# Performance work log

Hardware: AMD Instinct MI355X
Metric: run time of the kernel (lower is better)

## Reference

```python
import jax, jax.numpy as jnp
import numpy as np

B, LQ, S, D, H = 8, 1024, 256, 1024, 16
HD = D // H
LN_EPS = 1e-5


def layer_norm(x, g, b):
    m = jnp.mean(x, axis=-1, keepdims=True)
    v = jnp.mean((x - m) ** 2, axis=-1, keepdims=True)
    return (x - m) / jnp.sqrt(v + LN_EPS) * g + b


def setup_inputs() -> dict:
    key = jax.random.key(0)
    ks = jax.random.split(key, 12)
    sc = 0.02
    p = lambda k, shp: jax.random.normal(k, shp, dtype=jnp.float32) * sc
    return {
        "memory": jax.random.normal(ks[0], (B, LQ, D // 2), dtype=jnp.float32),
        "gaze_features": jax.random.normal(ks[1], (B, LQ, D // 2), dtype=jnp.float32),
        "text_features": jax.random.normal(ks[2], (B, S, D), dtype=jnp.float32),
        "w_in": p(ks[3], (3 * D, D)),  # packed q,k,v in_proj (torch MHA layout)
        "b_in": jnp.zeros((3 * D,), jnp.float32),
        "w_o": p(ks[4], (D, D)),
        "b_o": jnp.zeros((D,), jnp.float32),
        "w1": p(ks[5], (D, D)),
        "b1": jnp.zeros((D,), jnp.float32),
        "w2": p(ks[6], (D, D)),
        "b2": jnp.zeros((D,), jnp.float32),
        "g1": jnp.ones((D,), jnp.float32),
        "be1": jnp.zeros((D,), jnp.float32),
        "g2": jnp.ones((D,), jnp.float32),
        "be2": jnp.zeros((D,), jnp.float32),
    }


def reference(memory, gaze_features, text_features, w_in, b_in, w_o, b_o,
              w1, b1, w2, b2, g1, be1, g2, be2):
    combined = jnp.concatenate([memory, gaze_features], axis=-1)  # [B, LQ, D]
    wq, wk, wv = w_in[:D], w_in[D:2 * D], w_in[2 * D:]
    bq, bk, bv = b_in[:D], b_in[D:2 * D], b_in[2 * D:]

    q = (combined @ wq.T + bq).reshape(B, LQ, H, HD)
    k = (text_features @ wk.T + bk).reshape(B, S, H, HD)
    v = (text_features @ wv.T + bv).reshape(B, S, H, HD)

    scores = jnp.einsum("bqhd,bkhd->bhqk", q, k) / jnp.sqrt(jnp.float32(HD))
    attn_w = jax.nn.softmax(scores, axis=-1)
    ctx = jnp.einsum("bhqk,bkhd->bqhd", attn_w, v).reshape(B, LQ, D)
    attn_output = ctx @ w_o.T + b_o  # [B, LQ, D]

    # dual FFN branches share linear1/linear2 (as in the source); dropout = eval identity
    ffn = jax.nn.relu(attn_output @ w1.T + b1) @ w2.T + b2
    refpoint_embed = layer_norm(ffn, g1, be1)
    tgt = layer_norm(ffn, g2, be2)

    # vectorized box decode (replaces the per-element Python loop)
    s = jax.nn.sigmoid(attn_output[..., :4])
    xc, yc, w, h = s[..., 0], s[..., 1], s[..., 2], s[..., 3]
    init_box_proposal = jnp.stack(
        [xc - w / 2, yc - h / 2, xc + w / 2, yc + h / 2], axis=-1)  # [B, LQ, 4]

    return refpoint_embed, tgt, init_box_proposal
```

## Files before the change

kernel.cpp:

```cpp
#include <hip/hip_runtime.h>


typedef unsigned short u16;
typedef unsigned int u32;
typedef __bf16 bf16x8 __attribute__((ext_vector_type(8)));
typedef float f32x4 __attribute__((ext_vector_type(4)));
typedef u16 u16x4 __attribute__((ext_vector_type(4)));

struct CvtArgs { const void* in[15]; };

__device__ __forceinline__ u16 f2bf(float f) {
  u32 u = __builtin_bit_cast(u32, f);
  u += 0x7fffu + ((u >> 16) & 1u);
  return (u16)(u >> 16);
}
__device__ __forceinline__ float bf2f(u16 h) {
  u32 u = ((u32)h) << 16;
  return __builtin_bit_cast(float, u);
}

struct WsPtrs {
  u16 *c_mem, *c_gaze, *c_text, *c_win, *c_bin, *c_wo, *c_bo, *c_w1, *c_b1,
      *c_w2, *c_b2, *c_g1, *c_be1, *c_g2, *c_be2;
  u16 *q, *k, *v, *ctx, *woT, *wf, *bfb, *h1, *ffnb;
};
__device__ __forceinline__ WsPtrs wsp(u16* C) {
  WsPtrs w;
  w.c_mem = C;                 w.c_gaze = C + 4194304;   w.c_text = C + 8388608;
  w.c_win = C + 10485760;      w.c_bin = C + 13631488;   w.c_wo = C + 13634560;
  w.c_bo = C + 14683136;       w.c_w1 = C + 14684160;    w.c_b1 = C + 15732736;
  w.c_w2 = C + 15733760;       w.c_b2 = C + 16782336;    w.c_g1 = C + 16783360;
  w.c_be1 = C + 16784384;      w.c_g2 = C + 16785408;    w.c_be2 = C + 16786432;
  u16* B2 = C + 16787488;
  w.q = B2;                    w.k = B2 + 8388608;       w.v = B2 + 10485760;
  w.ctx = B2 + 12582912;
  w.woT = B2 + 20971520;
  w.wf  = B2 + 22020096;
  w.bfb = B2 + 23068672;
  w.h1  = B2 + 29360128;
  w.ffnb = B2;
  return w;
}

__device__ __forceinline__ void cvt_chunk(bool f32in, u16* dst,
                                          const void* const* srcs, u32 c8) {
  const u32 cum[16] = {0u, 4194304u, 8388608u, 10485760u, 13631488u, 13634560u,
                       14683136u, 14684160u, 15732736u, 15733760u, 16782336u,
                       16783360u, 16784384u, 16785408u, 16786432u, 16787456u};
  u32 base = c8 * 8u;
  int idx = 0;
#pragma unroll
  for (int i = 1; i < 15; ++i) if (base >= cum[i]) idx = i;
  u32 off = base - cum[idx];
  if (f32in) {
    const float* s = (const float*)srcs[idx] + off;
    float4 a = ((const float4*)s)[0];
    float4 b = ((const float4*)s)[1];
    u16 t[8] = {f2bf(a.x), f2bf(a.y), f2bf(a.z), f2bf(a.w),
                f2bf(b.x), f2bf(b.y), f2bf(b.z), f2bf(b.w)};
    *(uint4*)(dst + base) = *(const uint4*)t;
  } else {
    *(uint4*)(dst + base) = *(const uint4*)((const u16*)srcs[idx] + off);
  }
}

__global__ __launch_bounds__(256) void cvt_tr(CvtArgs a, u16* ws) {
  __shared__ u16 tile[128 * 136];
  const bool f32in = (((const u32*)a.in[11])[0] == 0x3F800000u);
  const int bid = blockIdx.x, tid = threadIdx.x;
  if (bid < 64) {
    WsPtrs w = wsp(ws);
    int tr = bid >> 3, tc = bid & 7;
#pragma unroll
    for (int p = 0; p < 8; ++p) {
      int t = p * 16 + (tid >> 4);
      int j8 = (tid & 15) * 8;
      u16 tmp[8];
      if (f32in) {
        const float* s = (const float*)a.in[5] + (size_t)(tr * 128 + t) * 1024 + tc * 128 + j8;
        float4 x = ((const float4*)s)[0], y = ((const float4*)s)[1];
        tmp[0]=f2bf(x.x); tmp[1]=f2bf(x.y); tmp[2]=f2bf(x.z); tmp[3]=f2bf(x.w);
        tmp[4]=f2bf(y.x); tmp[5]=f2bf(y.y); tmp[6]=f2bf(y.z); tmp[7]=f2bf(y.w);
      } else {
        *(uint4*)tmp = *(const uint4*)((const u16*)a.in[5] + (size_t)(tr * 128 + t) * 1024 + tc * 128 + j8);
      }
      *(uint4*)&tile[t * 136 + j8] = *(const uint4*)tmp;
    }
    __syncthreads();
#pragma unroll
    for (int p = 0; p < 8; ++p) {
      int j = p * 16 + (tid >> 4);
      int t8 = (tid & 15) * 8;
      u16 tmp[8];
#pragma unroll
      for (int i = 0; i < 8; ++i) tmp[i] = tile[(t8 + i) * 136 + j];
      *(uint4*)(w.woT + (size_t)(tc * 128 + j) * 1024 + tr * 128 + t8) = *(const uint4*)tmp;
    }
  } else {
    u32 c8 = (u32)(bid - 64) * 256u + tid;
    if (c8 < 2098432u) cvt_chunk(f32in, ws, a.in, c8);
  }
}

__device__ __forceinline__ void gemm_core(
    u16* sA, u16* sB,
    const u16* A0, const u16* A1, int Ksplit, int lda0, int lda1,
    const u16* W, const u16* bias, void* out, int N, int K,
    int mode, int lg, int m0, int n0)
{
  const int tid = threadIdx.x;
  const int wave = tid >> 6, lane = tid & 63;
  const int quad = lane >> 4, l16 = lane & 15;
  const int wm = wave >> 1, wn = wave & 1;

  f32x4 acc[4][4];
#pragma unroll
  for (int i = 0; i < 4; ++i)
#pragma unroll
    for (int j = 0; j < 4; ++j) acc[i][j] = (f32x4){0.f, 0.f, 0.f, 0.f};

  for (int k0 = 0; k0 < K; k0 += 64) {
#pragma unroll
    for (int qi = 0; qi < 4; ++qi) {
      int p = (wave * 4 + qi) * 64 + lane;
      int row = p >> 3;
      int c = (p & 7) ^ (row & 7);
      int gk = k0 + (c << 3);
      const u16* srcA = (gk < Ksplit) ? (A0 + (size_t)(m0 + row) * lda0 + gk)
                                      : (A1 + (size_t)(m0 + row) * lda1 + (gk - Ksplit));
      __builtin_amdgcn_global_load_lds(
          (const __attribute__((address_space(1))) void*)srcA,
          (__attribute__((address_space(3))) void*)&sA[(size_t)(wave * 4 + qi) * 512],
          16, 0, 0);
      const u16* srcB = W + (size_t)(n0 + row) * K + gk;
      __builtin_amdgcn_global_load_lds(
          (const __attribute__((address_space(1))) void*)srcB,
          (__attribute__((address_space(3))) void*)&sB[(size_t)(wave * 4 + qi) * 512],
          16, 0, 0);
    }
    __syncthreads();
#pragma unroll
    for (int ks = 0; ks < 2; ++ks) {
      const int ch = (ks << 2) + quad;
      bf16x8 af[4], bw[4];
#pragma unroll
      for (int i = 0; i < 4; ++i) {
        int row = wm * 64 + i * 16 + l16;
        af[i] = *(const bf16x8*)&sA[(row << 6) + ((ch ^ (row & 7)) << 3)];
      }
#pragma unroll
      for (int j = 0; j < 4; ++j) {
        int row = wn * 64 + j * 16 + l16;
        bw[j] = *(const bf16x8*)&sB[(row << 6) + ((ch ^ (row & 7)) << 3)];
      }
#pragma unroll
      for (int i = 0; i < 4; ++i)
#pragma unroll
        for (int j = 0; j < 4; ++j)
          acc[i][j] = __builtin_amdgcn_mfma_f32_16x16x32_bf16(af[i], bw[j], acc[i][j], 0, 0, 0);
    }
    __syncthreads();
  }

#pragma unroll
  for (int i = 0; i < 4; ++i) {
#pragma unroll
    for (int j = 0; j < 4; ++j) {
      int n = n0 + wn * 64 + j * 16 + l16;
      float bv = bias ? bf2f(bias[n]) : 0.f;
#pragma unroll
      for (int rr = 0; rr < 4; ++rr) {
        int m = m0 + wm * 64 + i * 16 + quad * 4 + rr;
        float val = acc[i][j][rr] + bv;
        if (mode == 1) val = fmaxf(val, 0.f);
        if (mode <= 1) {
          ((u16*)out)[(size_t)m * N + n] = f2bf(val);
        } else if (mode == 3) {
          int b = m >> lg, l = m & ((1 << lg) - 1);
          int h = n >> 6, d = n & 63;
          ((u16*)out)[((size_t)((b * 16 + h)) << (lg + 6)) + (l << 6) + d] = f2bf(val);
        } else {
          int b = m >> lg, s = m & ((1 << lg) - 1);
          int h = n >> 6, d = n & 63;
          ((u16*)out)[((size_t)(((b * 16 + h) << 6) + d) << lg) + s] = f2bf(val);
        }
      }
    }
  }
}

__global__ __launch_bounds__(256, 4) void qkvwf(u16* ws) {
  __shared__ __align__(16) u16 lds[16384];
  WsPtrs w = wsp(ws);
  const int bid = blockIdx.x, tid = threadIdx.x;
  if (bid < 512) {
    gemm_core(lds, lds + 8192, w.c_mem, w.c_gaze, 512, 512, 512,
              w.c_win, w.c_bin, w.q, 1024, 1024, 3, 10,
              (bid >> 3) * 128, (bid & 7) * 128);
  } else if (bid < 640) {
    int u = bid - 512;
    gemm_core(lds, lds + 8192, w.c_text, w.c_text, 1024, 1024, 1024,
              w.c_win + 1048576, w.c_bin + 1024, w.k, 1024, 1024, 3, 8,
              (u >> 3) * 128, (u & 7) * 128);
  } else if (bid < 768) {
    int u = bid - 640;
    gemm_core(lds, lds + 8192, w.c_text, w.c_text, 1024, 1024, 1024,
              w.c_win + 2097152, w.c_bin + 2048, w.v, 1024, 1024, 4, 8,
              (u >> 3) * 128, (u & 7) * 128);
  } else if (bid < 832) {
    int u = bid - 768;
    gemm_core(lds, lds + 8192, w.c_w1, w.c_w1, 1024, 1024, 1024,
              w.woT, nullptr, w.wf, 1024, 1024, 0, 0,
              (u >> 3) * 128, (u & 7) * 128);
  } else {
    int i = (bid - 832) * 256 + tid;
    const u16* w1row = w.c_w1 + (size_t)i * 1024;
    float acc = bf2f(w.c_b1[i]);
    for (int kk = 0; kk < 1024; kk += 8) {
      bf16x8 wv = *(const bf16x8*)(w1row + kk);
      bf16x8 bv = *(const bf16x8*)(w.c_bo + kk);
#pragma unroll
      for (int j = 0; j < 8; ++j) acc += (float)wv[j] * (float)bv[j];
    }
    w.bfb[i] = f2bf(acc);
  }
}

__global__ __launch_bounds__(256) void attn_kernel(u16* ws) {
  __shared__ u16 sV[64 * 256];
  __shared__ u16 sKP[256 * 64];
  WsPtrs w = wsp(ws);
  const int tid = threadIdx.x;
  const int wave = tid >> 6, lane = tid & 63;
  const int quad = lane >> 4, l16 = lane & 15;
  const int qb = blockIdx.x & 15, bh = blockIdx.x >> 4;

  {
    int rr = tid >> 3, c8 = (tid & 7) << 3;
    const u16* kb = w.k + (size_t)bh * 16384;
#pragma unroll
    for (int p = 0; p < 8; ++p) {
      int row = p * 32 + rr;
      uint4 val = *(const uint4*)(kb + row * 64 + c8);
      *(uint4*)&sKP[(row << 6) + ((((c8 >> 3) ^ (row & 7))) << 3)] = val;
    }
    int r2 = tid >> 5, c8b = (tid & 31) << 3;
    const u16* vb = w.v + (size_t)bh * 16384;
#pragma unroll
    for (int p = 0; p < 8; ++p) {
      int row = p * 8 + r2;
      uint4 val = *(const uint4*)(vb + (row << 8) + c8b);
      *(uint4*)&sV[(row << 8) + ((((c8b >> 3) ^ (row & 7))) << 3)] = val;
    }
  }
  bf16x8 aq[2];
  {
    const u16* qrow = w.q + ((size_t)bh * 1024 + qb * 64 + wave * 16 + l16) * 64 + quad * 8;
    aq[0] = *(const bf16x8*)(qrow);
    aq[1] = *(const bf16x8*)(qrow + 32);
  }
  __syncthreads();

  f32x4 sc[16];
#pragma unroll
  for (int nt = 0; nt < 16; ++nt) sc[nt] = (f32x4){0.f, 0.f, 0.f, 0.f};
#pragma unroll
  for (int ks = 0; ks < 2; ++ks) {
    const int ch = (ks << 2) + quad;
#pragma unroll
    for (int nt = 0; nt < 16; ++nt) {
      int row = nt * 16 + l16;
      bf16x8 bk = *(const bf16x8*)&sKP[(row << 6) + ((ch ^ (row & 7)) << 3)];
      sc[nt] = __builtin_amdgcn_mfma_f32_16x16x32_bf16(aq[ks], bk, sc[nt], 0, 0, 0);
    }
  }
#pragma unroll
  for (int rr = 0; rr < 4; ++rr) {
    float mx = -1e30f;
#pragma unroll
    for (int nt = 0; nt < 16; ++nt) mx = fmaxf(mx, sc[nt][rr]);
    for (int off = 1; off < 16; off <<= 1) mx = fmaxf(mx, __shfl_xor(mx, off, 64));
    float sum = 0.f;
#pragma unroll
    for (int nt = 0; nt < 16; ++nt) {
      float p = __expf((sc[nt][rr] - mx) * 0.125f);
      sc[nt][rr] = p; sum += p;
    }
    for (int off = 1; off < 16; off <<= 1) sum += __shfl_xor(sum, off, 64);
    float inv = 1.f / sum;
#pragma unroll
    for (int nt = 0; nt < 16; ++nt) sc[nt][rr] *= inv;
  }
  __syncthreads();
#pragma unroll
  for (int nt = 0; nt < 16; ++nt)
#pragma unroll
    for (int rr = 0; rr < 4; ++rr) {
      int row = wave * 16 + quad * 4 + rr;
      int col = nt * 16 + l16;
      sKP[(row << 8) + (((col >> 3) ^ (row & 7)) << 3) + (col & 7)] = f2bf(sc[nt][rr]);
    }
  __syncthreads();

  f32x4 o[4];
#pragma unroll
  for (int j = 0; j < 4; ++j) o[j] = (f32x4){0.f, 0.f, 0.f, 0.f};
#pragma unroll
  for (int ks = 0; ks < 8; ++ks) {
    const int ch = (ks << 2) + quad;
    int prow = wave * 16 + l16;
    bf16x8 ap = *(const bf16x8*)&sKP[(prow << 8) + ((ch ^ (prow & 7)) << 3)];
#pragma unroll
    for (int j = 0; j < 4; ++j) {
      int vrow = j * 16 + l16;
      bf16x8 bv = *(const bf16x8*)&sV[(vrow << 8) + ((ch ^ (vrow & 7)) << 3)];
      o[j] = __builtin_amdgcn_mfma_f32_16x16x32_bf16(ap, bv, o[j], 0, 0, 0);
    }
  }
  const int b = bh >> 4, h = bh & 15;
#pragma unroll
  for (int j = 0; j < 4; ++j)
#pragma unroll
    for (int rr = 0; rr < 4; ++rr) {
      int m = qb * 64 + wave * 16 + quad * 4 + rr;
      int d = h * 64 + j * 16 + l16;
      w.ctx[((size_t)b * 1024 + m) * 1024 + d] = f2bf(o[j][rr]);
    }
}

__global__ __launch_bounds__(256, 4) void h1box(u16* ws, void* out, const void* g1orig) {
  __shared__ __align__(16) u16 lds[16384];
  WsPtrs w = wsp(ws);
  const int u = blockIdx.x, tid = threadIdx.x;
  const int r16 = tid >> 4, l4 = tid & 15;
  {
    const bool f32out = (((const u32*)g1orig)[0] == 0x3F800000u);
    int m = u * 16 + r16;
    int k0 = l4 * 64;
    const u16* crow = w.ctx + (size_t)m * 1024 + k0;
    float a0 = 0.f, a1 = 0.f, a2 = 0.f, a3 = 0.f;
#pragma unroll
    for (int kk = 0; kk < 64; kk += 8) {
      bf16x8 cv = *(const bf16x8*)(crow + kk);
      bf16x8 w0 = *(const bf16x8*)(w.c_wo + k0 + kk);
      bf16x8 w1 = *(const bf16x8*)(w.c_wo + 1024 + k0 + kk);
      bf16x8 w2 = *(const bf16x8*)(w.c_wo + 2048 + k0 + kk);
      bf16x8 w3 = *(const bf16x8*)(w.c_wo + 3072 + k0 + kk);
#pragma unroll
      for (int j = 0; j < 8; ++j) {
        float c = (float)cv[j];
        a0 += c * (float)w0[j]; a1 += c * (float)w1[j];
        a2 += c * (float)w2[j]; a3 += c * (float)w3[j];
      }
    }
    for (int off = 1; off < 16; off <<= 1) {
      a0 += __shfl_xor(a0, off, 64); a1 += __shfl_xor(a1, off, 64);
      a2 += __shfl_xor(a2, off, 64); a3 += __shfl_xor(a3, off, 64);
    }
    if (l4 == 0) {
      a0 += bf2f(w.c_bo[0]); a1 += bf2f(w.c_bo[1]);
      a2 += bf2f(w.c_bo[2]); a3 += bf2f(w.c_bo[3]);
      float s0 = 1.f / (1.f + __expf(-a0)), s1 = 1.f / (1.f + __expf(-a1));
      float s2 = 1.f / (1.f + __expf(-a2)), s3 = 1.f / (1.f + __expf(-a3));
      float o0 = s0 - s2 * 0.5f, o1 = s1 - s3 * 0.5f;
      float o2 = s0 + s2 * 0.5f, o3 = s1 + s3 * 0.5f;
      if (f32out) {
        float* fo = (float*)out + 16777216;
        *(float4*)(fo + (size_t)m * 4) = make_float4(o0, o1, o2, o3);
      } else {
        u16* bo = (u16*)out + 16777216;
        u16x4 o; o[0] = f2bf(o0); o[1] = f2bf(o1); o[2] = f2bf(o2); o[3] = f2bf(o3);
        *(u16x4*)(bo + (size_t)m * 4) = o;
      }
    }
  }
  gemm_core(lds, lds + 8192, w.ctx, w.ctx, 1024, 1024, 1024,
            w.wf, w.bfb, w.h1, 1024, 1024, 1, 0, (u >> 3) * 128, (u & 7) * 128);
}

__global__ __launch_bounds__(256, 4) void w2gemm(u16* ws) {
  __shared__ __align__(16) u16 lds[16384];
  WsPtrs w = wsp(ws);
  gemm_core(lds, lds + 8192, w.h1, w.h1, 1024, 1024, 1024,
            w.c_w2, w.c_b2, w.ffnb, 1024, 1024, 0, 0,
            (blockIdx.x >> 3) * 128, (blockIdx.x & 7) * 128);
}

__global__ __launch_bounds__(256) void ln_kernel(u16* ws, void* outv, const void* g1orig) {
  WsPtrs w = wsp(ws);
  const bool f32out = (((const u32*)g1orig)[0] == 0x3F800000u);
  const int row = blockIdx.x, tid = threadIdx.x;
  int c = tid * 4;
  u16x4 xr = *(const u16x4*)(w.ffnb + (size_t)row * 1024 + c);
  float x[4] = {bf2f(xr[0]), bf2f(xr[1]), bf2f(xr[2]), bf2f(xr[3])};
  float s = x[0] + x[1] + x[2] + x[3];
  float s2 = x[0]*x[0] + x[1]*x[1] + x[2]*x[2] + x[3]*x[3];
  for (int m = 32; m >= 1; m >>= 1) { s += __shfl_xor(s, m, 64); s2 += __shfl_xor(s2, m, 64); }
  __shared__ float red[8];
  int wv = tid >> 6;
  if ((tid & 63) == 0) { red[wv] = s; red[4 + wv] = s2; }
  __syncthreads();
  s = red[0] + red[1] + red[2] + red[3];
  s2 = red[4] + red[5] + red[6] + red[7];
  float mean = s * (1.f / 1024.f);
  float var = s2 * (1.f / 1024.f) - mean * mean;
  float inv = rsqrtf(var + 1e-5f);
  float y[4] = {(x[0] - mean) * inv, (x[1] - mean) * inv, (x[2] - mean) * inv, (x[3] - mean) * inv};
  float v1[4], v2[4];
#pragma unroll
  for (int i = 0; i < 4; ++i) {
    v1[i] = y[i] * bf2f(w.c_g1[c + i]) + bf2f(w.c_be1[c + i]);
    v2[i] = y[i] * bf2f(w.c_g2[c + i]) + bf2f(w.c_be2[c + i]);
  }
  if (f32out) {
    float* fo = (float*)outv;
    *(float4*)(fo + (size_t)row * 1024 + c) = make_float4(v1[0], v1[1], v1[2], v1[3]);
    *(float4*)(fo + 8388608 + (size_t)row * 1024 + c) = make_float4(v2[0], v2[1], v2[2], v2[3]);
  } else {
    u16* out = (u16*)outv;
    u16x4 o1, o2;
#pragma unroll
    for (int i = 0; i < 4; ++i) { o1[i] = f2bf(v1[i]); o2[i] = f2bf(v2[i]); }
    *(u16x4*)(out + (size_t)row * 1024 + c) = o1;
    *(u16x4*)(out + 8388608 + (size_t)row * 1024 + c) = o2;
  }
}

extern "C" void kernel_launch(void* const* d_in, const int* in_sizes, int n_in,
                              void* d_out, int out_size, void* d_ws, size_t ws_size,
                              hipStream_t stream) {
  CvtArgs ca;
  for (int i = 0; i < 15; ++i) ca.in[i] = d_in[i];
  u16* ws = (u16*)d_ws;
  dim3 blk(256);
  cvt_tr<<<dim3(8261), blk, 0, stream>>>(ca, ws);
  qkvwf<<<dim3(836), blk, 0, stream>>>(ws);
  attn_kernel<<<dim3(2048), blk, 0, stream>>>(ws);
  h1box<<<dim3(512), blk, 0, stream>>>(ws, d_out, d_in[11]);
  w2gemm<<<dim3(512), blk, 0, stream>>>(ws);
  ln_kernel<<<dim3(8192), blk, 0, stream>>>(ws, d_out, d_in[11]);
}
```

Before: 300.3 us.

## Template GEMM tile width, swizzle block order, read K/V directly in attention

```diff
diff --git a/kernel.cpp b/kernel.cpp
--- a/kernel.cpp
+++ b/kernel.cpp
@@ -102,22 +102,25 @@
   }
 }
 
+template <int TN>
 __device__ __forceinline__ void gemm_core(
     u16* sA, u16* sB,
     const u16* A0, const u16* A1, int Ksplit, int lda0, int lda1,
     const u16* W, const u16* bias, void* out, int N, int K,
     int mode, int lg, int m0, int n0)
 {
+  constexpr int JN = TN >> 5;
+  constexpr int BCPT = TN >> 5;
   const int tid = threadIdx.x;
   const int wave = tid >> 6, lane = tid & 63;
   const int quad = lane >> 4, l16 = lane & 15;
   const int wm = wave >> 1, wn = wave & 1;
 
-  f32x4 acc[4][4];
+  f32x4 acc[4][JN];
 #pragma unroll
   for (int i = 0; i < 4; ++i)
 #pragma unroll
-    for (int j = 0; j < 4; ++j) acc[i][j] = (f32x4){0.f, 0.f, 0.f, 0.f};
+    for (int j = 0; j < JN; ++j) acc[i][j] = (f32x4){0.f, 0.f, 0.f, 0.f};
 
   for (int k0 = 0; k0 < K; k0 += 64) {
 #pragma unroll
@@ -132,31 +135,38 @@
           (const __attribute__((address_space(1))) void*)srcA,
           (__attribute__((address_space(3))) void*)&sA[(size_t)(wave * 4 + qi) * 512],
           16, 0, 0);
+    }
+#pragma unroll
+    for (int qi = 0; qi < BCPT; ++qi) {
+      int p = (wave * BCPT + qi) * 64 + lane;
+      int row = p >> 3;
+      int c = (p & 7) ^ (row & 7);
+      int gk = k0 + (c << 3);
       const u16* srcB = W + (size_t)(n0 + row) * K + gk;
       __builtin_amdgcn_global_load_lds(
           (const __attribute__((address_space(1))) void*)srcB,
-          (__attribute__((address_space(3))) void*)&sB[(size_t)(wave * 4 + qi) * 512],
+          (__attribute__((address_space(3))) void*)&sB[(size_t)(wave * BCPT + qi) * 512],
           16, 0, 0);
     }
     __syncthreads();
 #pragma unroll
     for (int ks = 0; ks < 2; ++ks) {
       const int ch = (ks << 2) + quad;
-      bf16x8 af[4], bw[4];
+      bf16x8 af[4], bw[JN];
 #pragma unroll
       for (int i = 0; i < 4; ++i) {
         int row = wm * 64 + i * 16 + l16;
         af[i] = *(const bf16x8*)&sA[(row << 6) + ((ch ^ (row & 7)) << 3)];
       }
 #pragma unroll
-      for (int j = 0; j < 4; ++j) {
-        int row = wn * 64 + j * 16 + l16;
+      for (int j = 0; j < JN; ++j) {
+        int row = wn * (TN >> 1) + j * 16 + l16;
         bw[j] = *(const bf16x8*)&sB[(row << 6) + ((ch ^ (row & 7)) << 3)];
       }
 #pragma unroll
       for (int i = 0; i < 4; ++i)
 #pragma unroll
-        for (int j = 0; j < 4; ++j)
+        for (int j = 0; j < JN; ++j)
           acc[i][j] = __builtin_amdgcn_mfma_f32_16x16x32_bf16(af[i], bw[j], acc[i][j], 0, 0, 0);
     }
     __syncthreads();
@@ -165,8 +175,8 @@
 #pragma unroll
   for (int i = 0; i < 4; ++i) {
 #pragma unroll
-    for (int j = 0; j < 4; ++j) {
-      int n = n0 + wn * 64 + j * 16 + l16;
+    for (int j = 0; j < JN; ++j) {
+      int n = n0 + wn * (TN >> 1) + j * 16 + l16;
       float bv = bias ? bf2f(bias[n]) : 0.f;
 #pragma unroll
       for (int rr = 0; rr < 4; ++rr) {
@@ -189,29 +199,34 @@
   }
 }
 
+__device__ __forceinline__ int xswz(int u, int n8) {
+  return (u & 7) * n8 + (u >> 3);
+}
+
 __global__ __launch_bounds__(256, 4) void qkvwf(u16* ws) {
   __shared__ __align__(16) u16 lds[16384];
   WsPtrs w = wsp(ws);
   const int bid = blockIdx.x, tid = threadIdx.x;
   if (bid < 512) {
-    gemm_core(lds, lds + 8192, w.c_mem, w.c_gaze, 512, 512, 512,
-              w.c_win, w.c_bin, w.q, 1024, 1024, 3, 10,
-              (bid >> 3) * 128, (bid & 7) * 128);
+    int u = xswz(bid, 64);
+    gemm_core<128>(lds, lds + 8192, w.c_mem, w.c_gaze, 512, 512, 512,
+                   w.c_win, w.c_bin, w.q, 1024, 1024, 3, 10,
+                   (u >> 3) * 128, (u & 7) * 128);
   } else if (bid < 640) {
-    int u = bid - 512;
-    gemm_core(lds, lds + 8192, w.c_text, w.c_text, 1024, 1024, 1024,
-              w.c_win + 1048576, w.c_bin + 1024, w.k, 1024, 1024, 3, 8,
-              (u >> 3) * 128, (u & 7) * 128);
+    int u = xswz(bid - 512, 16);
+    gemm_core<128>(lds, lds + 8192, w.c_text, w.c_text, 1024, 1024, 1024,
+                   w.c_win + 1048576, w.c_bin + 1024, w.k, 1024, 1024, 3, 8,
+                   (u >> 3) * 128, (u & 7) * 128);
   } else if (bid < 768) {
-    int u = bid - 640;
-    gemm_core(lds, lds + 8192, w.c_text, w.c_text, 1024, 1024, 1024,
-              w.c_win + 2097152, w.c_bin + 2048, w.v, 1024, 1024, 4, 8,
-              (u >> 3) * 128, (u & 7) * 128);
+    int u = xswz(bid - 640, 16);
+    gemm_core<128>(lds, lds + 8192, w.c_text, w.c_text, 1024, 1024, 1024,
+                   w.c_win + 2097152, w.c_bin + 2048, w.v, 1024, 1024, 4, 8,
+                   (u >> 3) * 128, (u & 7) * 128);
   } else if (bid < 832) {
-    int u = bid - 768;
-    gemm_core(lds, lds + 8192, w.c_w1, w.c_w1, 1024, 1024, 1024,
-              w.woT, nullptr, w.wf, 1024, 1024, 0, 0,
-              (u >> 3) * 128, (u & 7) * 128);
+    int u = xswz(bid - 768, 8);
+    gemm_core<128>(lds, lds + 8192, w.c_w1, w.c_w1, 1024, 1024, 1024,
+                   w.woT, nullptr, w.wf, 1024, 1024, 0, 0,
+                   (u >> 3) * 128, (u & 7) * 128);
   } else {
     int i = (bid - 832) * 256 + tid;
     const u16* w1row = w.c_w1 + (size_t)i * 1024;
@@ -226,54 +241,39 @@
   }
 }
 
-__global__ __launch_bounds__(256) void attn_kernel(u16* ws) {
-  __shared__ u16 sV[64 * 256];
-  __shared__ u16 sKP[256 * 64];
+__global__ __launch_bounds__(256, 4) void attn_kernel(u16* ws) {
+  __shared__ u16 sP[64 * 256];
   WsPtrs w = wsp(ws);
   const int tid = threadIdx.x;
   const int wave = tid >> 6, lane = tid & 63;
   const int quad = lane >> 4, l16 = lane & 15;
-  const int qb = blockIdx.x & 15, bh = blockIdx.x >> 4;
-
-  {
-    int rr = tid >> 3, c8 = (tid & 7) << 3;
-    const u16* kb = w.k + (size_t)bh * 16384;
-#pragma unroll
-    for (int p = 0; p < 8; ++p) {
-      int row = p * 32 + rr;
-      uint4 val = *(const uint4*)(kb + row * 64 + c8);
-      *(uint4*)&sKP[(row << 6) + ((((c8 >> 3) ^ (row & 7))) << 3)] = val;
-    }
-    int r2 = tid >> 5, c8b = (tid & 31) << 3;
-    const u16* vb = w.v + (size_t)bh * 16384;
-#pragma unroll
-    for (int p = 0; p < 8; ++p) {
-      int row = p * 8 + r2;
-      uint4 val = *(const uint4*)(vb + (row << 8) + c8b);
-      *(uint4*)&sV[(row << 8) + ((((c8b >> 3) ^ (row & 7))) << 3)] = val;
-    }
-  }
+  const int su = xswz(blockIdx.x, 256);
+  const int qb = su & 15, bh = su >> 4;
+  const u16* kb = w.k + (size_t)bh * 16384;
+  const u16* vb = w.v + (size_t)bh * 16384;
+
   bf16x8 aq[2];
   {
     const u16* qrow = w.q + ((size_t)bh * 1024 + qb * 64 + wave * 16 + l16) * 64 + quad * 8;
     aq[0] = *(const bf16x8*)(qrow);
     aq[1] = *(const bf16x8*)(qrow + 32);
   }
-  __syncthreads();
 
   f32x4 sc[16];
 #pragma unroll
   for (int nt = 0; nt < 16; ++nt) sc[nt] = (f32x4){0.f, 0.f, 0.f, 0.f};
+  __builtin_amdgcn_s_setprio(1);
 #pragma unroll
   for (int ks = 0; ks < 2; ++ks) {
     const int ch = (ks << 2) + quad;
 #pragma unroll
     for (int nt = 0; nt < 16; ++nt) {
       int row = nt * 16 + l16;
-      bf16x8 bk = *(const bf16x8*)&sKP[(row << 6) + ((ch ^ (row & 7)) << 3)];
+      bf16x8 bk = *(const bf16x8*)(kb + (size_t)row * 64 + ch * 8);
       sc[nt] = __builtin_amdgcn_mfma_f32_16x16x32_bf16(aq[ks], bk, sc[nt], 0, 0, 0);
     }
   }
+  __builtin_amdgcn_s_setprio(0);
 #pragma unroll
   for (int rr = 0; rr < 4; ++rr) {
     float mx = -1e30f;
@@ -291,32 +291,33 @@
 #pragma unroll
     for (int nt = 0; nt < 16; ++nt) sc[nt][rr] *= inv;
   }
-  __syncthreads();
 #pragma unroll
   for (int nt = 0; nt < 16; ++nt)
 #pragma unroll
     for (int rr = 0; rr < 4; ++rr) {
       int row = wave * 16 + quad * 4 + rr;
       int col = nt * 16 + l16;
-      sKP[(row << 8) + (((col >> 3) ^ (row & 7)) << 3) + (col & 7)] = f2bf(sc[nt][rr]);
+      sP[(row << 8) + (((col >> 3) ^ (row & 7)) << 3) + (col & 7)] = f2bf(sc[nt][rr]);
     }
   __syncthreads();
 
   f32x4 o[4];
 #pragma unroll
   for (int j = 0; j < 4; ++j) o[j] = (f32x4){0.f, 0.f, 0.f, 0.f};
+  __builtin_amdgcn_s_setprio(1);
 #pragma unroll
   for (int ks = 0; ks < 8; ++ks) {
     const int ch = (ks << 2) + quad;
     int prow = wave * 16 + l16;
-    bf16x8 ap = *(const bf16x8*)&sKP[(prow << 8) + ((ch ^ (prow & 7)) << 3)];
+    bf16x8 ap = *(const bf16x8*)&sP[(prow << 8) + ((ch ^ (prow & 7)) << 3)];
 #pragma unroll
     for (int j = 0; j < 4; ++j) {
       int vrow = j * 16 + l16;
-      bf16x8 bv = *(const bf16x8*)&sV[(vrow << 8) + ((ch ^ (vrow & 7)) << 3)];
+      bf16x8 bv = *(const bf16x8*)(vb + (size_t)vrow * 256 + ch * 8);
       o[j] = __builtin_amdgcn_mfma_f32_16x16x32_bf16(ap, bv, o[j], 0, 0, 0);
     }
   }
+  __builtin_amdgcn_s_setprio(0);
   const int b = bh >> 4, h = bh & 15;
 #pragma unroll
   for (int j = 0; j < 4; ++j)
@@ -329,35 +330,35 @@
 }
 
 __global__ __launch_bounds__(256, 4) void h1box(u16* ws, void* out, const void* g1orig) {
-  __shared__ __align__(16) u16 lds[16384];
+  __shared__ __align__(16) u16 lds[12288];
   WsPtrs w = wsp(ws);
   const int u = blockIdx.x, tid = threadIdx.x;
-  const int r16 = tid >> 4, l4 = tid & 15;
   {
     const bool f32out = (((const u32*)g1orig)[0] == 0x3F800000u);
-    int m = u * 16 + r16;
-    int k0 = l4 * 64;
+    int m = u * 8 + (tid >> 5);
+    int l32 = tid & 31;
+    int k0 = l32 * 32;
     const u16* crow = w.ctx + (size_t)m * 1024 + k0;
     float a0 = 0.f, a1 = 0.f, a2 = 0.f, a3 = 0.f;
 #pragma unroll
-    for (int kk = 0; kk < 64; kk += 8) {
+    for (int kk = 0; kk < 32; kk += 8) {
       bf16x8 cv = *(const bf16x8*)(crow + kk);
       bf16x8 w0 = *(const bf16x8*)(w.c_wo + k0 + kk);
-      bf16x8 w1 = *(const bf16x8*)(w.c_wo + 1024 + k0 + kk);
-      bf16x8 w2 = *(const bf16x8*)(w.c_wo + 2048 + k0 + kk);
-      bf16x8 w3 = *(const bf16x8*)(w.c_wo + 3072 + k0 + kk);
+      bf16x8 w1v = *(const bf16x8*)(w.c_wo + 1024 + k0 + kk);
+      bf16x8 w2v = *(const bf16x8*)(w.c_wo + 2048 + k0 + kk);
+      bf16x8 w3v = *(const bf16x8*)(w.c_wo + 3072 + k0 + kk);
 #pragma unroll
       for (int j = 0; j < 8; ++j) {
         float c = (float)cv[j];
-        a0 += c * (float)w0[j]; a1 += c * (float)w1[j];
-        a2 += c * (float)w2[j]; a3 += c * (float)w3[j];
-      }
-    }
-    for (int off = 1; off < 16; off <<= 1) {
+        a0 += c * (float)w0[j]; a1 += c * (float)w1v[j];
+        a2 += c * (float)w2v[j]; a3 += c * (float)w3v[j];
+      }
+    }
+    for (int off = 1; off < 32; off <<= 1) {
       a0 += __shfl_xor(a0, off, 64); a1 += __shfl_xor(a1, off, 64);
       a2 += __shfl_xor(a2, off, 64); a3 += __shfl_xor(a3, off, 64);
     }
-    if (l4 == 0) {
+    if (l32 == 0) {
       a0 += bf2f(w.c_bo[0]); a1 += bf2f(w.c_bo[1]);
       a2 += bf2f(w.c_bo[2]); a3 += bf2f(w.c_bo[3]);
       float s0 = 1.f / (1.f + __expf(-a0)), s1 = 1.f / (1.f + __expf(-a1));
@@ -374,16 +375,19 @@
       }
     }
   }
-  gemm_core(lds, lds + 8192, w.ctx, w.ctx, 1024, 1024, 1024,
-            w.wf, w.bfb, w.h1, 1024, 1024, 1, 0, (u >> 3) * 128, (u & 7) * 128);
+  int us = xswz(u, 128);
+  gemm_core<64>(lds, lds + 8192, w.ctx, w.ctx, 1024, 1024, 1024,
+                w.wf, w.bfb, w.h1, 1024, 1024, 1, 0,
+                (us >> 4) * 128, (us & 15) * 64);
 }
 
 __global__ __launch_bounds__(256, 4) void w2gemm(u16* ws) {
-  __shared__ __align__(16) u16 lds[16384];
+  __shared__ __align__(16) u16 lds[12288];
   WsPtrs w = wsp(ws);
-  gemm_core(lds, lds + 8192, w.h1, w.h1, 1024, 1024, 1024,
-            w.c_w2, w.c_b2, w.ffnb, 1024, 1024, 0, 0,
-            (blockIdx.x >> 3) * 128, (blockIdx.x & 7) * 128);
+  int us = xswz((int)blockIdx.x, 128);
+  gemm_core<64>(lds, lds + 8192, w.h1, w.h1, 1024, 1024, 1024,
+                w.c_w2, w.c_b2, w.ffnb, 1024, 1024, 0, 0,
+                (us >> 4) * 128, (us & 15) * 64);
 }
 
 __global__ __launch_bounds__(256) void ln_kernel(u16* ws, void* outv, const void* g1orig) {
@@ -436,7 +440,7 @@
   cvt_tr<<<dim3(8261), blk, 0, stream>>>(ca, ws);
   qkvwf<<<dim3(836), blk, 0, stream>>>(ws);
   attn_kernel<<<dim3(2048), blk, 0, stream>>>(ws);
-  h1box<<<dim3(512), blk, 0, stream>>>(ws, d_out, d_in[11]);
-  w2gemm<<<dim3(512), blk, 0, stream>>>(ws);
+  h1box<<<dim3(1024), blk, 0, stream>>>(ws, d_out, d_in[11]);
+  w2gemm<<<dim3(1024), blk, 0, stream>>>(ws);
   ln_kernel<<<dim3(8192), blk, 0, stream>>>(ws, d_out, d_in[11]);
 }
```

Measured after the change: 331.8 us. 1.1x slower.
